# Kernel optimization log

Measured on AMD Instinct MI355X. Metric: run time of the kernel, lower is better.

The kernel has to match this reference:

```python
import jax, jax.numpy as jnp
import numpy as np

NUM_HEADS = 8
DIM_HEAD_QK = 32
DIM_HEAD_V = 32
BLOCK = 8
HALO = 3
WIN = BLOCK + 2 * HALO  # 14
SCALE = DIM_HEAD_QK ** -0.5


def rel_logits_1d(q, rel_k, permute_mask):
    N, H, W, d = q.shape
    rel_size = rel_k.shape[0]
    win = (rel_size + 1) // 2
    x = jnp.einsum('nhwd,rd->nhwr', q, rel_k)
    x = x.reshape(N * H, W, rel_size)
    x = jnp.pad(x, ((0, 0), (0, 0), (0, 1))).reshape(N * H, -1)
    x = jnp.pad(x, ((0, 0), (0, rel_size - W)))
    x = x.reshape(N * H, W + 1, rel_size)[:, :W, win - 1:]
    x = jnp.broadcast_to(x.reshape(N, H, 1, W, win), (N, H, win, W, win))
    return jnp.transpose(x, permute_mask)


def pos_embed_rel(q, height_rel, width_rel):
    BH, NB, HW, d = q.shape
    qb = q.reshape(-1, BLOCK, BLOCK, d)
    rel_w = rel_logits_1d(qb, width_rel, (0, 1, 3, 2, 4))
    rel_h = rel_logits_1d(jnp.swapaxes(qb, 1, 2), height_rel, (0, 3, 1, 4, 2))
    return (rel_h + rel_w).reshape(BH, NB, HW, WIN * WIN)


def reference(x, q_weight, kv_weight, height_rel, width_rel):
    B, C, H, W = x.shape
    nhb, nwb = H // BLOCK, W // BLOCK
    nb = nhb * nwb
    # 1x1 conv projections
    q = jnp.einsum('bchw,oc->bohw', x, q_weight)
    q = q.reshape(B * NUM_HEADS, DIM_HEAD_QK, nhb, BLOCK, nwb, BLOCK)
    q = jnp.transpose(q, (0, 1, 3, 5, 2, 4)).reshape(B * NUM_HEADS, DIM_HEAD_QK, BLOCK * BLOCK, nb)
    q = jnp.swapaxes(q, 1, 3)  # (BH, nb, BLOCK*BLOCK, dhq)
    kv = jnp.einsum('bchw,oc->bohw', x, kv_weight)
    kv = jnp.pad(kv, ((0, 0), (0, 0), (HALO, HALO), (HALO, HALO)))
    # halo windows: overlapping WINxWIN patches strided by BLOCK
    h_idx = jnp.arange(nhb)[:, None] * BLOCK + jnp.arange(WIN)[None, :]
    w_idx = jnp.arange(nwb)[:, None] * BLOCK + jnp.arange(WIN)[None, :]
    kv = kv[:, :, h_idx, :][:, :, :, :, w_idx]
    kv = jnp.transpose(kv, (0, 1, 2, 4, 3, 5)).reshape(
        B * NUM_HEADS, DIM_HEAD_QK + DIM_HEAD_V, nb, WIN * WIN)
    kv = jnp.transpose(kv, (0, 2, 3, 1))
    k, v = kv[..., :DIM_HEAD_QK], kv[..., DIM_HEAD_QK:]
    attn = jnp.einsum('bnqd,bnkd->bnqk', q, k) * SCALE
    attn = attn + pos_embed_rel(q, height_rel, width_rel)
    attn = jax.nn.softmax(attn, axis=-1)
    out = jnp.einsum('bnqk,bnkd->bnqd', attn, v)
    out = jnp.swapaxes(out, 1, 3)  # (BH, dhv, BLOCK*BLOCK, nb)
    out = out.reshape(-1, BLOCK, BLOCK, nhb, nwb)
    out = jnp.transpose(out, (0, 3, 1, 4, 2)).reshape(B, NUM_HEADS * DIM_HEAD_V, H, W)
    return out


def setup_inputs() -> dict:
    key = jax.random.key(0)
    k1, k2, k3, k4, k5 = jax.random.split(key, 5)
    dim = 256
    std = dim ** -0.5
    x = jax.random.normal(k1, (8, 256, 96, 96), dtype=jnp.float32)
    q_weight = jax.random.normal(k2, (256, 256), dtype=jnp.float32) * std
    kv_weight = jax.random.normal(k3, (512, 256), dtype=jnp.float32) * std
    height_rel = jax.random.normal(k4, (2 * WIN - 1, DIM_HEAD_QK), dtype=jnp.float32) * SCALE
    width_rel = jax.random.normal(k5, (2 * WIN - 1, DIM_HEAD_QK), dtype=jnp.float32) * SCALE
    return {'x': x, 'q_weight': q_weight, 'kv_weight': kv_weight,
            'height_rel': height_rel, 'width_rel': width_rel}
```

## Files before the change

### kernel.cpp

```cpp
#include <hip/hip_runtime.h>
#include <math.h>

#define NPIX 9216
#define SCALE 0.17677669529663687f
#define LOG2E 1.4426950408889634f

typedef __attribute__((ext_vector_type(8))) short bh8;
typedef __attribute__((ext_vector_type(4))) float f4;

__device__ __forceinline__ unsigned short f2bf(float f) {
    unsigned u = __float_as_uint(f);
    u += 0x7fff + ((u >> 16) & 1);
    return (unsigned short)(u >> 16);
}
__device__ __forceinline__ void gload_lds16(const void* g, void* l) {
    __builtin_amdgcn_global_load_lds(
        (const __attribute__((address_space(1))) unsigned int*)g,
        (__attribute__((address_space(3))) unsigned int*)l, 16, 0, 0);
}

__global__ void wconv_kernel(const float* __restrict__ qw, const float* __restrict__ kvw,
                             const float* __restrict__ hrel, const float* __restrict__ wrel,
                             unsigned short* __restrict__ Wb,
                             unsigned short* __restrict__ relb) {
    int bid = blockIdx.x, tid = threadIdx.x;
    if (bid < 768) {
        float v = (bid < 256) ? qw[bid * 256 + tid] : kvw[(bid - 256) * 256 + tid];
        Wb[bid * 256 + tid] = f2bf(v);
    } else {
        int e = (bid - 768) * 256 + tid;
        int half = e >> 10, r = (e >> 5) & 31, d = e & 31;
        float v = 0.0f;
        if (r < 27) v = (half ? wrel : hrel)[r * 32 + d] * LOG2E;
        relb[half * 1024 + r * 32 + d] = f2bf(v);
    }
}

__global__ __launch_bounds__(256) void xtrans_kernel(const float* __restrict__ x,
                                                     unsigned short* __restrict__ xt) {
    int b = blockIdx.z;
    int p0 = blockIdx.x * 128, c0 = blockIdx.y * 128;
    int tid = threadIdx.x;
    __shared__ __align__(16) unsigned short ts[128 * 136];
    const float* xb = x + (size_t)b * 256 * NPIX;
    #pragma unroll
    for (int it = 0; it < 16; ++it) {
        int e = it * 256 + tid;
        int ch = e >> 5, p4 = (e & 31) * 4;
        float4 v = *(const float4*)(xb + (size_t)(c0 + ch) * NPIX + p0 + p4);
        ts[(p4 + 0) * 136 + ch] = f2bf(v.x);
        ts[(p4 + 1) * 136 + ch] = f2bf(v.y);
        ts[(p4 + 2) * 136 + ch] = f2bf(v.z);
        ts[(p4 + 3) * 136 + ch] = f2bf(v.w);
    }
    __syncthreads();
    unsigned short* xtb = xt + (size_t)b * NPIX * 256;
    #pragma unroll
    for (int it = 0; it < 8; ++it) {
        int e = it * 256 + tid;
        int p = e >> 4, ck = (e & 15) * 8;
        *(int4*)(xtb + (size_t)(p0 + p) * 256 + c0 + ck) = *(const int4*)&ts[p * 136 + ck];
    }
}

__global__ __launch_bounds__(256) void proj_kernel(const unsigned short* __restrict__ xt,
                                                   const unsigned short* __restrict__ Wb,
                                                   unsigned short* __restrict__ qb,
                                                   unsigned short* __restrict__ kvb) {
    int flat = blockIdx.x + 72 * (blockIdx.y + 6 * blockIdx.z);
    int w = (flat & 7) * 432 + (flat >> 3);
    int n0 = (w % 6) * 128;
    int m0 = ((w / 6) % 72) * 128;
    int b  = w / 432;
    int tid = threadIdx.x, lane = tid & 63, wave = tid >> 6;
    int ll = lane & 15;
    __shared__ __align__(16) char smem[34816];
    char* As = smem;
    char* Bs = smem + 16384;
    const unsigned short* xtb = xt + (size_t)b * NPIX * 256;

    f4 acc[4][4] = {};
    int wm = (wave & 1) * 64, wn = (wave >> 1) * 64;

    for (int k0 = 0; k0 < 256; k0 += 64) {
        __syncthreads();
        #pragma unroll
        for (int i = 0; i < 4; ++i) {
            int c = wave * 4 + i;
            gload_lds16(xtb + (size_t)(m0 + c * 8 + (lane >> 3)) * 256 + k0 + (lane & 7) * 8,
                        As + c * 1024);
            gload_lds16(Wb + (size_t)(n0 + c * 8 + (lane >> 3)) * 256 + k0 + (lane & 7) * 8,
                        Bs + c * 1024);
        }
        __syncthreads();
        #pragma unroll
        for (int ks = 0; ks < 2; ++ks) {
            bh8 af[4], bf[4];
            #pragma unroll
            for (int i = 0; i < 4; ++i)
                af[i] = *(const bh8*)(As + (wm + i * 16 + ll) * 128 + ks * 64 + (lane >> 4) * 16);
            #pragma unroll
            for (int j = 0; j < 4; ++j)
                bf[j] = *(const bh8*)(Bs + (wn + j * 16 + ll) * 128 + ks * 64 + (lane >> 4) * 16);
            #pragma unroll
            for (int i = 0; i < 4; ++i)
                #pragma unroll
                for (int j = 0; j < 4; ++j)
                    acc[i][j] = __builtin_amdgcn_mfma_f32_16x16x32_bf16(af[i], bf[j], acc[i][j], 0, 0, 0);
        }
    }

    __syncthreads();
    unsigned short* ts = (unsigned short*)smem;
    int q4 = (lane >> 4) * 4;
    #pragma unroll
    for (int i = 0; i < 4; ++i) {
        #pragma unroll
        for (int j = 0; j < 4; ++j) {
            int ch = wn + j * 16 + ll;
            #pragma unroll
            for (int r = 0; r < 4; ++r)
                ts[(wm + i * 16 + q4 + r) * 136 + ch] = f2bf(acc[i][j][r]);
        }
    }
    __syncthreads();
    bool isQ = (n0 < 256);
    #pragma unroll
    for (int it = 0; it < 8; ++it) {
        int e = it * 256 + tid;
        int pixl = e >> 4, ck = (e & 15) * 8;
        int4 v = *(const int4*)&ts[pixl * 136 + ck];
        int pix = m0 + pixl, ch = n0 + ck;
        if (isQ) {
            int head = ch >> 5, d = ch & 31;
            *(int4*)&qb[((size_t)(b * 8 + head) * NPIX + pix) * 32 + d] = v;
        } else {
            int c = ch - 256, head = c >> 6, dv = c & 63;
            *(int4*)&kvb[((size_t)(b * 8 + head) * NPIX + pix) * 64 + dv] = v;
        }
    }
}

__global__ __launch_bounds__(256) void attn_kernel(const unsigned short* __restrict__ qbuf,
                                                   const unsigned short* __restrict__ kvbuf,
                                                   const unsigned short* __restrict__ relb,
                                                   float* __restrict__ out) {
    int flat = blockIdx.x + 144 * blockIdx.y;
    int w = (flat & 7) * 1152 + (flat >> 3);
    int nbid = w % 144, bh = w / 144;
    int b = bh >> 3, head = bh & 7;
    int hb = nbid / 12, wblk = nbid % 12;
    int r0 = hb * 8, c0 = wblk * 8;
    int tid = threadIdx.x, lane = tid & 63, wave = tid >> 6;
    int ll = lane & 15, lq = lane >> 4;
    int m0 = wave * 16;

    __shared__ __align__(16) char smem[45312];
    unsigned short* Vt = (unsigned short*)smem;
    char* strip = smem + 15360 + wave * 7424;
    float*          RhTw = (float*)strip;
    float*          Rww  = (float*)(strip + 2240);
    unsigned short* Ps   = (unsigned short*)strip;
    float*          smR  = (float*)(smem + 45056);

    const unsigned short* qb  = qbuf  + (size_t)bh * NPIX * 32;
    const unsigned short* kvb = kvbuf + (size_t)bh * NPIX * 64;

    int qp0 = m0 + ll;
    int pixq = (r0 + (qp0 >> 3)) * 96 + c0 + (qp0 & 7);
    bh8 aq = *(const bh8*)&qb[(size_t)pixq * 32 + lq * 8];

    #pragma unroll
    for (int it = 0; it < 2; ++it) {
        int e = it * 256 + tid;
        int part = e >> 7, kp2 = e & 127;
        if (kp2 < 112) {
            int a = kp2 >> 3, b2 = (kp2 & 7) * 2;
            int gr = r0 + a - 3, gc = c0 + b2 - 3;
            int4 lo = {0, 0, 0, 0}, hi = {0, 0, 0, 0};
            bool rok = ((kp2 & 7) < 7) && ((unsigned)gr < 96u);
            if (rok && (unsigned)gc < 96u)
                lo = *(const int4*)&kvb[(size_t)(gr * 96 + gc) * 64 + 32 + part * 8];
            if (rok && (unsigned)(gc + 1) < 96u)
                hi = *(const int4*)&kvb[(size_t)(gr * 96 + gc + 1) * 64 + 32 + part * 8];
            int g = kp2 >> 2, kb = b2 & 7;
            const unsigned* lw = (const unsigned*)&lo;
            const unsigned* hw = (const unsigned*)&hi;
            #pragma unroll
            for (int jw = 0; jw < 4; ++jw) {
                unsigned l2 = lw[jw], h2 = hw[jw];
                unsigned v0 = (l2 & 0xffffu) | (h2 << 16);
                unsigned v1 = (l2 >> 16) | (h2 & 0xffff0000u);
                int d0 = part * 8 + jw * 2;
                int s0 = (((jw * 2) & 3) + part) & 3;
                int s1 = (((jw * 2 + 1) & 3) + part) & 3;
                *(unsigned*)&Vt[d0 * 240 + ((g ^ s0) * 8) + kb] = v0;
                *(unsigned*)&Vt[(d0 + 1) * 240 + ((g ^ s1) * 8) + kb] = v1;
            }
        }
    }

    f4 zero4 = {0.f, 0.f, 0.f, 0.f};
    #pragma unroll
    for (int t = 0; t < 2; ++t) {
        int r = t * 16 + ll;
        bh8 hbv = *(const bh8*)&relb[(size_t)r * 32 + lq * 8];
        bh8 wbv = *(const bh8*)&relb[1024 + (size_t)r * 32 + lq * 8];
        f4 ch = __builtin_amdgcn_mfma_f32_16x16x32_bf16(aq, hbv, zero4, 0, 0, 0);
        f4 cw = __builtin_amdgcn_mfma_f32_16x16x32_bf16(aq, wbv, zero4, 0, 0, 0);
        if (r < 28) *(f4*)&RhTw[r * 20 + lq * 4] = ch;
        if (r >= 6 && r < 27) {
            #pragma unroll
            for (int rr = 0; rr < 4; ++rr)
                Rww[(lq * 4 + rr) * 23 + (r - 6)] = cw[rr];
        }
    }

    int gcq = c0 + ll - 3;
    bool lane_ok = (ll < 14) && ((unsigned)gcq < 96u);
    const unsigned short* kcol = kvb + (size_t)gcq * 64 + lq * 8;
    f4 S[14];
    #pragma unroll
    for (int t = 0; t < 14; ++t) {
        int gr = r0 + t - 3;
        bh8 bk = {};
        if (lane_ok && (unsigned)gr < 96u)
            bk = *(const bh8*)(kcol + (size_t)gr * 96 * 64);
        S[t] = __builtin_amdgcn_mfma_f32_16x16x32_bf16(aq, bk, zero4, 0, 0, 0);
    }

    int row0 = m0 + lq * 4;
    int h = row0 >> 3;
    bool valid = (ll < 14);
    float rw4[4];
    #pragma unroll
    for (int rr = 0; rr < 4; ++rr) {
        int row = row0 + rr;
        rw4[rr] = valid ? Rww[(lq * 4 + rr) * 23 + 7 + ll - (row & 7)] : -INFINITY;
    }
    const float SL = SCALE * LOG2E;
    float sm4[4] = {0.f, 0.f, 0.f, 0.f};
    #pragma unroll
    for (int t = 0; t < 14; ++t) {
        f4 rh = *(const f4*)&RhTw[(13 + t - h) * 20 + lq * 4];
        #pragma unroll
        for (int rr = 0; rr < 4; ++rr) {
            float lg = S[t][rr] * SL + rh[rr] + rw4[rr];
            float p = __builtin_amdgcn_exp2f(lg);
            S[t][rr] = p;
            sm4[rr] += p;
        }
    }
    #pragma unroll
    for (int rr = 0; rr < 4; ++rr) {
        sm4[rr] += __shfl_xor(sm4[rr], 1);
        sm4[rr] += __shfl_xor(sm4[rr], 2);
        sm4[rr] += __shfl_xor(sm4[rr], 4);
        sm4[rr] += __shfl_xor(sm4[rr], 8);
    }
    if (ll == 0) {
        #pragma unroll
        for (int rr = 0; rr < 4; ++rr) smR[row0 + rr] = sm4[rr];
    }

    __syncthreads();

    #pragma unroll
    for (int t = 0; t < 14; ++t) {
        int col = t * 16 + ll;
        #pragma unroll
        for (int rr = 0; rr < 4; ++rr)
            Ps[(lq * 4 + rr) * 232 + col] = f2bf(S[t][rr]);
    }

    f4 O[2] = {zero4, zero4};
    #pragma unroll
    for (int kt = 0; kt < 7; ++kt) {
        bh8 bp = *(const bh8*)&Ps[ll * 232 + kt * 32 + lq * 8];
        #pragma unroll
        for (int mt = 0; mt < 2; ++mt) {
            int d = mt * 16 + ll;
            int s = ((d & 3) + ((d >> 3) & 3)) & 3;
            bh8 av = *(const bh8*)&Vt[d * 240 + (((kt * 4 + lq) ^ s) * 8)];
            O[mt] = __builtin_amdgcn_mfma_f32_16x16x32_bf16(av, bp, O[mt], 0, 0, 0);
        }
    }

    int qp = m0 + ll;
    float rs = 1.0f / smR[qp];
    int pix = (r0 + (qp >> 3)) * 96 + c0 + (qp & 7);
    float* ob = out + (size_t)(b * 256 + head * 32) * NPIX;
    #pragma unroll
    for (int mt = 0; mt < 2; ++mt) {
        #pragma unroll
        for (int rr = 0; rr < 4; ++rr) {
            int d = mt * 16 + lq * 4 + rr;
            ob[(size_t)d * NPIX + pix] = O[mt][rr] * rs;
        }
    }
}

extern "C" void kernel_launch(void* const* d_in, const int* in_sizes, int n_in,
                              void* d_out, int out_size, void* d_ws, size_t ws_size,
                              hipStream_t stream) {
    const float* x    = (const float*)d_in[0];
    const float* qw   = (const float*)d_in[1];
    const float* kvw  = (const float*)d_in[2];
    const float* hrel = (const float*)d_in[3];
    const float* wrel = (const float*)d_in[4];
    float* out = (float*)d_out;

    char* ws = (char*)d_ws;
    unsigned short* xt    = (unsigned short*)ws;
    unsigned short* Wb    = (unsigned short*)(ws + 37748736);
    unsigned short* relb  = (unsigned short*)(ws + 38141952);
    unsigned short* qbuf  = (unsigned short*)(ws + 38146048);
    unsigned short* kvbuf = (unsigned short*)(ws + 75894784);

    wconv_kernel<<<dim3(776), 256, 0, stream>>>(qw, kvw, hrel, wrel, Wb, relb);
    xtrans_kernel<<<dim3(72, 2, 8), 256, 0, stream>>>(x, xt);
    proj_kernel<<<dim3(72, 6, 8), 256, 0, stream>>>(xt, Wb, qbuf, kvbuf);
    attn_kernel<<<dim3(144, 64), 256, 0, stream>>>(qbuf, kvbuf, relb, out);
}
```

Baseline: 301.9 us.

## Stage halo K tile in LDS and shrink shared memory for higher occupancy

The 14x14 halo K window is now loaded cooperatively into an LDS tile with coalesced 16-byte loads, and the QK^T MFMAs read from LDS. Previously each lane fetched strided K rows directly from global memory. The Ks buffer is aliased with the per-wave strips after a barrier. The P tile is written and consumed in two chunks, and the V transpose stride is shortened. Together these cut LDS from about 45 KB to about 32 KB, and launch_bounds now requests 4 blocks. The cost is two extra block barriers and tighter register and LDS budgets, which could cause spills or new bank conflicts.

```diff
diff --git a/kernel.cpp b/kernel.cpp
--- a/kernel.cpp
+++ b/kernel.cpp
@@ -141,10 +141,10 @@
     }
 }
 
-__global__ __launch_bounds__(256) void attn_kernel(const unsigned short* __restrict__ qbuf,
-                                                   const unsigned short* __restrict__ kvbuf,
-                                                   const unsigned short* __restrict__ relb,
-                                                   float* __restrict__ out) {
+__global__ __launch_bounds__(256, 4) void attn_kernel(const unsigned short* __restrict__ qbuf,
+                                                      const unsigned short* __restrict__ kvbuf,
+                                                      const unsigned short* __restrict__ relb,
+                                                      float* __restrict__ out) {
     int flat = blockIdx.x + 144 * blockIdx.y;
     int w = (flat & 7) * 1152 + (flat >> 3);
     int nbid = w % 144, bh = w / 144;
@@ -155,13 +155,14 @@
     int ll = lane & 15, lq = lane >> 4;
     int m0 = wave * 16;
 
-    __shared__ __align__(16) char smem[45312];
+    __shared__ __align__(16) char smem[32512];
     unsigned short* Vt = (unsigned short*)smem;
-    char* strip = smem + 15360 + wave * 7424;
+    unsigned short* Ks = (unsigned short*)(smem + 14336);
+    char* strip = smem + 14336 + wave * 4352;
     float*          RhTw = (float*)strip;
     float*          Rww  = (float*)(strip + 2240);
     unsigned short* Ps   = (unsigned short*)strip;
-    float*          smR  = (float*)(smem + 45056);
+    float*          smR  = (float*)(smem + 32256);
 
     const unsigned short* qb  = qbuf  + (size_t)bh * NPIX * 32;
     const unsigned short* kvb = kvbuf + (size_t)bh * NPIX * 64;
@@ -169,6 +170,16 @@
     int qp0 = m0 + ll;
     int pixq = (r0 + (qp0 >> 3)) * 96 + c0 + (qp0 & 7);
     bh8 aq = *(const bh8*)&qb[(size_t)pixq * 32 + lq * 8];
+
+    for (int e = tid; e < 896; e += 256) {
+        int kp = e >> 2, part = e & 3;
+        int a = kp >> 4, b2 = kp & 15;
+        int gr = r0 + a - 3, gc = c0 + b2 - 3;
+        int4 v = {0, 0, 0, 0};
+        if (b2 < 14 && (unsigned)gr < 96u && (unsigned)gc < 96u)
+            v = *(const int4*)&kvb[(size_t)(gr * 96 + gc) * 64 + part * 8];
+        *(int4*)&Ks[kp * 40 + part * 8] = v;
+    }
 
     #pragma unroll
     for (int it = 0; it < 2; ++it) {
@@ -194,13 +205,24 @@
                 int d0 = part * 8 + jw * 2;
                 int s0 = (((jw * 2) & 3) + part) & 3;
                 int s1 = (((jw * 2 + 1) & 3) + part) & 3;
-                *(unsigned*)&Vt[d0 * 240 + ((g ^ s0) * 8) + kb] = v0;
-                *(unsigned*)&Vt[(d0 + 1) * 240 + ((g ^ s1) * 8) + kb] = v1;
+                *(unsigned*)&Vt[d0 * 224 + ((g ^ s0) * 8) + kb] = v0;
+                *(unsigned*)&Vt[(d0 + 1) * 224 + ((g ^ s1) * 8) + kb] = v1;
             }
         }
     }
 
+    __syncthreads();
+
     f4 zero4 = {0.f, 0.f, 0.f, 0.f};
+    f4 S[14];
+    #pragma unroll
+    for (int t = 0; t < 14; ++t) {
+        bh8 bk = *(const bh8*)&Ks[(t * 16 + ll) * 40 + lq * 8];
+        S[t] = __builtin_amdgcn_mfma_f32_16x16x32_bf16(aq, bk, zero4, 0, 0, 0);
+    }
+
+    __syncthreads();
+
     #pragma unroll
     for (int t = 0; t < 2; ++t) {
         int r = t * 16 + ll;
@@ -216,19 +238,6 @@
         }
     }
 
-    int gcq = c0 + ll - 3;
-    bool lane_ok = (ll < 14) && ((unsigned)gcq < 96u);
-    const unsigned short* kcol = kvb + (size_t)gcq * 64 + lq * 8;
-    f4 S[14];
-    #pragma unroll
-    for (int t = 0; t < 14; ++t) {
-        int gr = r0 + t - 3;
-        bh8 bk = {};
-        if (lane_ok && (unsigned)gr < 96u)
-            bk = *(const bh8*)(kcol + (size_t)gr * 96 * 64);
-        S[t] = __builtin_amdgcn_mfma_f32_16x16x32_bf16(aq, bk, zero4, 0, 0, 0);
-    }
-
     int row0 = m0 + lq * 4;
     int h = row0 >> 3;
     bool valid = (ll < 14);
@@ -263,26 +272,34 @@
         for (int rr = 0; rr < 4; ++rr) smR[row0 + rr] = sm4[rr];
     }
 
-    __syncthreads();
-
-    #pragma unroll
-    for (int t = 0; t < 14; ++t) {
-        int col = t * 16 + ll;
-        #pragma unroll
-        for (int rr = 0; rr < 4; ++rr)
-            Ps[(lq * 4 + rr) * 232 + col] = f2bf(S[t][rr]);
-    }
-
     f4 O[2] = {zero4, zero4};
     #pragma unroll
-    for (int kt = 0; kt < 7; ++kt) {
-        bh8 bp = *(const bh8*)&Ps[ll * 232 + kt * 32 + lq * 8];
-        #pragma unroll
-        for (int mt = 0; mt < 2; ++mt) {
-            int d = mt * 16 + ll;
-            int s = ((d & 3) + ((d >> 3) & 3)) & 3;
-            bh8 av = *(const bh8*)&Vt[d * 240 + (((kt * 4 + lq) ^ s) * 8)];
-            O[mt] = __builtin_amdgcn_mfma_f32_16x16x32_bf16(av, bp, O[mt], 0, 0, 0);
+    for (int c = 0; c < 2; ++c) {
+        const int nt = c ? 6 : 8;
+        #pragma unroll
+        for (int tl = 0; tl < 8; ++tl) {
+            if (tl < nt) {
+                int t = c * 8 + tl;
+                int col = tl * 16 + ll;
+                #pragma unroll
+                for (int rr = 0; rr < 4; ++rr)
+                    Ps[(lq * 4 + rr) * 136 + col] = f2bf(S[t][rr]);
+            }
+        }
+        const int nkt = c ? 3 : 4;
+        #pragma unroll
+        for (int ktl = 0; ktl < 4; ++ktl) {
+            if (ktl < nkt) {
+                int kt = c * 4 + ktl;
+                bh8 bp = *(const bh8*)&Ps[ll * 136 + ktl * 32 + lq * 8];
+                #pragma unroll
+                for (int mt = 0; mt < 2; ++mt) {
+                    int d = mt * 16 + ll;
+                    int s = ((d & 3) + ((d >> 3) & 3)) & 3;
+                    bh8 av = *(const bh8*)&Vt[d * 224 + (((kt * 4 + lq) ^ s) * 8)];
+                    O[mt] = __builtin_amdgcn_mfma_f32_16x16x32_bf16(av, bp, O[mt], 0, 0, 0);
+                }
+            }
         }
     }
 
```

Result: faster. 258.5 us (-14.4%).
